# Performance work log

Measured on AMD Instinct MI355X. Metric: run time of the kernel, lower is better.

Reference implementation:

```python
import jax, jax.numpy as jnp
import numpy as np

N, D_IN, D_OUT = 500000, 128, 128
DROP_P = 0.5


def setup_inputs() -> dict:
    key = jax.random.key(0)
    k1, k2, k3, k4 = jax.random.split(key, 4)
    x = jax.random.normal(k1, (N, D_IN), dtype=jnp.float32)
    weight = jax.random.normal(k2, (D_IN, D_OUT), dtype=jnp.float32)
    support = jax.random.normal(k3, (D_OUT, D_OUT), dtype=jnp.float32)
    # inverted-dropout mask: Bernoulli(keep=1-p) scaled by 1/(1-p), matching F.dropout in training mode
    keep = 1.0 - DROP_P
    u = jax.random.uniform(k4, (N, D_IN), dtype=jnp.float32)
    drop_mask = (u < keep).astype(jnp.float32) / keep
    return {"x": x, "weight": weight, "support": support, "drop_mask": drop_mask}


def reference(x, weight, support, drop_mask):
    # training-mode dropout (deterministic mask), dense transform, right-multiply by support, ReLU
    xd = x * drop_mask                      # [N, D_IN]
    xw = jnp.matmul(xd, weight)             # [N, D_OUT]
    out = jnp.matmul(xw, support)           # [N, D_OUT]
    return jax.nn.relu(out)
```

## Files before the change

kernel.cpp:

```cpp
#include <hip/hip_runtime.h>
#include <hip/hip_bf16.h>


#define D 128
#define LDS_PITCH 136

typedef __attribute__((ext_vector_type(8))) short short8;
typedef __attribute__((ext_vector_type(4))) float f32x4;

__device__ __forceinline__ short f2bf(float f) {
    union { __hip_bfloat16 h; short s; } u;
    u.h = __float2bfloat16(f);
    return u.s;
}

__global__ void wprod_kernel(const float* __restrict__ weight,
                             const float* __restrict__ support,
                             unsigned short* __restrict__ wt) {
    __shared__ float wrow[D];
    const int i = blockIdx.x;
    const int j = threadIdx.x;
    wrow[j] = weight[i * D + j];
    __syncthreads();
    float acc = 0.f;
#pragma unroll 8
    for (int k = 0; k < D; ++k)
        acc = fmaf(wrow[k], support[k * D + j], acc);
    union { __hip_bfloat16 h; unsigned short s; } u;
    u.h = __float2bfloat16(acc);
    wt[(size_t)j * D + i] = u.s;
}

__global__ __launch_bounds__(256, 4) void gcn_fused(
    const float* __restrict__ x, const float* __restrict__ mask,
    const unsigned short* __restrict__ wt, float* __restrict__ out,
    int nslabs) {
    __shared__ __align__(16) unsigned short lw[D * LDS_PITCH];

    const uint4* src = reinterpret_cast<const uint4*>(wt);
    for (int c = threadIdx.x; c < 2048; c += 256) {
        const int n = c >> 4;
        const int kc = (c & 15) << 3;
        *reinterpret_cast<uint4*>(&lw[n * LDS_PITCH + kc]) = src[c];
    }
    __syncthreads();

    const int lane = threadIdx.x & 63;
    const int m = lane & 15;
    const int quad = lane >> 4;

    const int wave = (blockIdx.x * blockDim.x + threadIdx.x) >> 6;
    const int nwaves = (gridDim.x * blockDim.x) >> 6;

    for (int s = wave; s < nslabs; s += nwaves) {
        const float* xr = x + ((size_t)s * 16 + m) * D + quad * 8;
        const float* mr = mask + ((size_t)s * 16 + m) * D + quad * 8;

        short8 a[4];
#pragma unroll
        for (int kk = 0; kk < 4; ++kk) {
            f32x4 x0 = *reinterpret_cast<const f32x4*>(xr + kk * 32);
            f32x4 x1 = *reinterpret_cast<const f32x4*>(xr + kk * 32 + 4);
            f32x4 m0 = *reinterpret_cast<const f32x4*>(mr + kk * 32);
            f32x4 m1 = *reinterpret_cast<const f32x4*>(mr + kk * 32 + 4);
            f32x4 p0 = x0 * m0;
            f32x4 p1 = x1 * m1;
            short8 v;
            v[0] = f2bf(p0[0]); v[1] = f2bf(p0[1]);
            v[2] = f2bf(p0[2]); v[3] = f2bf(p0[3]);
            v[4] = f2bf(p1[0]); v[5] = f2bf(p1[1]);
            v[6] = f2bf(p1[2]); v[7] = f2bf(p1[3]);
            a[kk] = v;
        }

        float* orow = out + (size_t)s * 16 * D;
#pragma unroll
        for (int n = 0; n < 8; ++n) {
            f32x4 acc = {0.f, 0.f, 0.f, 0.f};
#pragma unroll
            for (int kk = 0; kk < 4; ++kk) {
                const short8 b = *reinterpret_cast<const short8*>(
                    &lw[(n * 16 + m) * LDS_PITCH + kk * 32 + quad * 8]);
                acc = __builtin_amdgcn_mfma_f32_16x16x32_bf16(a[kk], b, acc, 0, 0, 0);
            }
#pragma unroll
            for (int r = 0; r < 4; ++r) {
                const float v = acc[r];
                orow[(quad * 4 + r) * D + n * 16 + m] = v > 0.f ? v : 0.f;
            }
        }
    }
}

extern "C" void kernel_launch(void* const* d_in, const int* in_sizes, int n_in,
                              void* d_out, int out_size, void* d_ws, size_t ws_size,
                              hipStream_t stream) {
    const float* x = (const float*)d_in[0];
    const float* weight = (const float*)d_in[1];
    const float* support = (const float*)d_in[2];
    const float* mask = (const float*)d_in[3];
    float* out = (float*)d_out;
    unsigned short* wt = (unsigned short*)d_ws;

    const int nrows = in_sizes[0] / D;
    const int nslabs = nrows / 16;

    wprod_kernel<<<dim3(D), dim3(D), 0, stream>>>(weight, support, wt);
    gcn_fused<<<dim3(2048), dim3(256), 0, stream>>>(x, mask, wt, out, nslabs);
}
```

Measured before the change: 647.1 us.

## Prefetch next slab, swap MFMA operands for vector stores, pre-swizzle LDS weights

Loads of x and mask for the next slab are now issued before the current slab's MFMAs run, so global-load latency overlaps with compute. The MFMA operands are swapped so each lane holds four consecutive output columns. That allows 16-byte vectorised stores in place of scalar strided stores. The weight tile is stored in LDS in a fragment-linear layout so each B read is a conflict-free contiguous short8. The price is more VGPRs for the 16 prefetched float4 registers, which could lower occupancy under launch_bounds(256,4).

```diff
diff --git a/kernel.cpp b/kernel.cpp
--- a/kernel.cpp
+++ b/kernel.cpp
@@ -3,7 +3,6 @@
 
 
 #define D 128
-#define LDS_PITCH 136
 
 typedef __attribute__((ext_vector_type(8))) short short8;
 typedef __attribute__((ext_vector_type(4))) float f32x4;
@@ -35,36 +34,53 @@
     const float* __restrict__ x, const float* __restrict__ mask,
     const unsigned short* __restrict__ wt, float* __restrict__ out,
     int nslabs) {
-    __shared__ __align__(16) unsigned short lw[D * LDS_PITCH];
+    __shared__ __align__(16) unsigned short lw[8 * 4 * 64 * 8];
 
-    const uint4* src = reinterpret_cast<const uint4*>(wt);
-    for (int c = threadIdx.x; c < 2048; c += 256) {
-        const int n = c >> 4;
-        const int kc = (c & 15) << 3;
-        *reinterpret_cast<uint4*>(&lw[n * LDS_PITCH + kc]) = src[c];
+    {
+        const uint4* src = reinterpret_cast<const uint4*>(wt);
+        uint4* dst = reinterpret_cast<uint4*>(lw);
+        for (int f = threadIdx.x; f < 2048; f += 256) {
+            const int n = f >> 8;
+            const int kk = (f >> 6) & 3;
+            const int l = f & 63;
+            const int q = l >> 4, m = l & 15;
+            dst[f] = src[((n * 16 + m) * D + kk * 32 + q * 8) >> 3];
+        }
     }
     __syncthreads();
 
     const int lane = threadIdx.x & 63;
     const int m = lane & 15;
-    const int quad = lane >> 4;
+    const int q = lane >> 4;
 
     const int wave = (blockIdx.x * blockDim.x + threadIdx.x) >> 6;
     const int nwaves = (gridDim.x * blockDim.x) >> 6;
 
-    for (int s = wave; s < nslabs; s += nwaves) {
-        const float* xr = x + ((size_t)s * 16 + m) * D + quad * 8;
-        const float* mr = mask + ((size_t)s * 16 + m) * D + quad * 8;
+    const short8* bfr = reinterpret_cast<const short8*>(lw) + lane;
 
+    f32x4 xv[8], mv[8];
+
+#define ISSUE_LOADS(ss)                                                        \
+    do {                                                                       \
+        const float* xr_ = x + ((size_t)(ss) * 16 + m) * D + q * 8;            \
+        const float* mr_ = mask + ((size_t)(ss) * 16 + m) * D + q * 8;         \
+        _Pragma("unroll") for (int kk = 0; kk < 4; ++kk) {                     \
+            xv[kk * 2]     = *reinterpret_cast<const f32x4*>(xr_ + kk * 32);   \
+            xv[kk * 2 + 1] = *reinterpret_cast<const f32x4*>(xr_ + kk * 32 + 4);\
+            mv[kk * 2]     = *reinterpret_cast<const f32x4*>(mr_ + kk * 32);   \
+            mv[kk * 2 + 1] = *reinterpret_cast<const f32x4*>(mr_ + kk * 32 + 4);\
+        }                                                                      \
+    } while (0)
+
+    int s = wave;
+    if (s < nslabs) ISSUE_LOADS(s);
+
+    for (; s < nslabs; s += nwaves) {
         short8 a[4];
 #pragma unroll
         for (int kk = 0; kk < 4; ++kk) {
-            f32x4 x0 = *reinterpret_cast<const f32x4*>(xr + kk * 32);
-            f32x4 x1 = *reinterpret_cast<const f32x4*>(xr + kk * 32 + 4);
-            f32x4 m0 = *reinterpret_cast<const f32x4*>(mr + kk * 32);
-            f32x4 m1 = *reinterpret_cast<const f32x4*>(mr + kk * 32 + 4);
-            f32x4 p0 = x0 * m0;
-            f32x4 p1 = x1 * m1;
+            const f32x4 p0 = xv[kk * 2] * mv[kk * 2];
+            const f32x4 p1 = xv[kk * 2 + 1] * mv[kk * 2 + 1];
             short8 v;
             v[0] = f2bf(p0[0]); v[1] = f2bf(p0[1]);
             v[2] = f2bf(p0[2]); v[3] = f2bf(p0[3]);
@@ -73,23 +89,26 @@
             a[kk] = v;
         }
 
-        float* orow = out + (size_t)s * 16 * D;
+        const int s2 = s + nwaves;
+        if (s2 < nslabs) ISSUE_LOADS(s2);
+
+        float* orow = out + ((size_t)s * 16 + m) * D + q * 4;
 #pragma unroll
         for (int n = 0; n < 8; ++n) {
             f32x4 acc = {0.f, 0.f, 0.f, 0.f};
 #pragma unroll
-            for (int kk = 0; kk < 4; ++kk) {
-                const short8 b = *reinterpret_cast<const short8*>(
-                    &lw[(n * 16 + m) * LDS_PITCH + kk * 32 + quad * 8]);
-                acc = __builtin_amdgcn_mfma_f32_16x16x32_bf16(a[kk], b, acc, 0, 0, 0);
-            }
-#pragma unroll
-            for (int r = 0; r < 4; ++r) {
-                const float v = acc[r];
-                orow[(quad * 4 + r) * D + n * 16 + m] = v > 0.f ? v : 0.f;
-            }
+            for (int kk = 0; kk < 4; ++kk)
+                acc = __builtin_amdgcn_mfma_f32_16x16x32_bf16(
+                    bfr[(n * 4 + kk) * 64], a[kk], acc, 0, 0, 0);
+            f32x4 r;
+            r[0] = fmaxf(acc[0], 0.f);
+            r[1] = fmaxf(acc[1], 0.f);
+            r[2] = fmaxf(acc[2], 0.f);
+            r[3] = fmaxf(acc[3], 0.f);
+            *reinterpret_cast<f32x4*>(orow + n * 16) = r;
         }
     }
+#undef ISSUE_LOADS
 }
 
 extern "C" void kernel_launch(void* const* d_in, const int* in_sizes, int n_in,
```

Measured after the change: 821.9 us. 27.0% more time.
